# Performance work log

Measured on AMD Instinct MI355X. Metric: run time of the kernel, lower is better.

## Reference

```python
import jax, jax.numpy as jnp
import numpy as np

B, S = 32, 10  # hard-coded in original call()/reshape


def setup_inputs() -> dict:
    key = jax.random.key(0)
    k1, k2, k3 = jax.random.split(key, 3)
    D, K = 4096, 8192
    p = jax.random.normal(k1, (B, S, D), dtype=jnp.float32)
    q = jax.random.normal(k2, (B, S, D), dtype=jnp.float32)
    W = jax.random.uniform(k3, (K, D), dtype=jnp.float32)  # 'uniform' initializer
    return {"p": p, "q": q, "W": W}


def reference(p, q, W):
    # Multi-perspective matching: for each perspective k, weight p rows and the
    # last q state by W[k], then cosine distance = -mean(l2norm(a)*l2norm(b)).
    # Vectorized over (batch, perspective, seq) via einsums on W^2 -- never
    # materializes the (B,K,S,D) weighted tensors.
    D = p.shape[-1]
    W2 = W * W                                   # (K, D)
    q_last = q[:, -1, :]                          # (B, D)
    # dot(w*q_last, w*p_s) = sum_d p*q_last*W^2
    dot = jnp.einsum('bsd,kd->bks', p * q_last[:, None, :], W2)   # (B, K, S)
    norm_p = jnp.sqrt(jnp.einsum('bsd,kd->bks', p * p, W2))       # (B, K, S)
    norm_q = jnp.sqrt(jnp.einsum('bd,kd->bk', q_last * q_last, W2))  # (B, K)
    dist = -dot / (norm_p * norm_q[:, :, None] * D)  # -mean of normalized product
    # original concatenates over k then s per batch, then reshapes to (32,10,K)
    return dist.reshape(B, S, -1)
```

## Files before the change

kernel.cpp:

```cpp
#include <hip/hip_runtime.h>
#include <stdint.h>

#define B_ 32
#define S_ 10
#define D_ 4096
#define K_ 8192
#define RPB 21
#define M_REAL (B_ * RPB)

#define BM 128
#define BN 128
#define BK 32
#define M_PAD_MF 768
#define KSPLIT 2
#define KHALF (D_ / KSPLIT)

typedef _Float16 f16x8 __attribute__((ext_vector_type(8)));
typedef float f32x4 __attribute__((ext_vector_type(4)));
typedef unsigned short us4 __attribute__((ext_vector_type(4)));

__device__ __forceinline__ void async16(const void* g, void* l) {
  __builtin_amdgcn_global_load_lds(
      (const __attribute__((address_space(1))) unsigned int*)g,
      (__attribute__((address_space(3))) unsigned int*)l, 16, 0, 0);
}

__global__ __launch_bounds__(256)
void build_a_f16(const float* __restrict__ p, const float* __restrict__ q,
                 unsigned short* __restrict__ Af) {
  size_t idx = (size_t)blockIdx.x * 256 + threadIdx.x;
  int d4 = (int)(idx & 1023);
  int m = (int)(idx >> 10);
  float4 v = make_float4(0.f, 0.f, 0.f, 0.f);
  if (m < M_REAL) {
    int b = m / RPB;
    int r = m - b * RPB;
    const float4* q4 = (const float4*)(q + (size_t)(b * S_ + (S_ - 1)) * D_);
    if (r < S_) {
      const float4* p4 = (const float4*)(p + (size_t)(b * S_ + r) * D_);
      float4 pv = p4[d4]; float4 qv = q4[d4];
      v = make_float4(pv.x * qv.x, pv.y * qv.y, pv.z * qv.z, pv.w * qv.w);
    } else if (r < 2 * S_) {
      const float4* p4 = (const float4*)(p + (size_t)(b * S_ + (r - S_)) * D_);
      float4 pv = p4[d4];
      v = make_float4(pv.x * pv.x, pv.y * pv.y, pv.z * pv.z, pv.w * pv.w);
    } else {
      float4 qv = q4[d4];
      v = make_float4(qv.x * qv.x, qv.y * qv.y, qv.z * qv.z, qv.w * qv.w);
    }
  }
  us4 h;
  ((unsigned short*)&h)[0] = (unsigned short)__builtin_bit_cast(unsigned short, (_Float16)v.x);
  ((unsigned short*)&h)[1] = (unsigned short)__builtin_bit_cast(unsigned short, (_Float16)v.y);
  ((unsigned short*)&h)[2] = (unsigned short)__builtin_bit_cast(unsigned short, (_Float16)v.z);
  ((unsigned short*)&h)[3] = (unsigned short)__builtin_bit_cast(unsigned short, (_Float16)v.w);
  ((us4*)Af)[idx] = h;
}

__global__ __launch_bounds__(256)
void gemm_mfma(const unsigned short* __restrict__ Af, const float* __restrict__ W,
               float* __restrict__ G) {
  __shared__ unsigned short lds[2 * 128 * 32];
  const int tid = threadIdx.x;
  const int lane = tid & 63;
  const int wid = tid >> 6;
  const int m0 = blockIdx.y * BM;
  const int n0 = blockIdx.x * BN;
  const int ks = blockIdx.z;
  const int d_base = ks * KHALF;

  const unsigned short* gpA[2];
  uint32_t ldsoffA[2];
#pragma unroll
  for (int half = 0; half < 2; ++half) {
    int row = half * 64 + wid * 16 + (lane >> 2);
    int k16l = (lane & 3) ^ ((row ^ (row >> 2)) & 3);
    gpA[half] = Af + (size_t)(m0 + row) * D_ + d_base + k16l * 8;
    ldsoffA[half] = (uint32_t)(half * 4096 + wid * 1024);
  }

  const int wrow = tid >> 1;
  const int wh = tid & 1;
  const float* gW = W + (size_t)(n0 + wrow) * D_ + d_base + wh * 16;
  const int wsz = (wrow ^ (wrow >> 2)) & 3;
  char* const ldsb = (char*)lds;
  char* const ldsWb = ldsb + 8192;
  const uint32_t wbyte0 = (uint32_t)(wrow * 64 + ((2 * wh) ^ wsz) * 16);
  const uint32_t wbyte1 = (uint32_t)(wrow * 64 + ((2 * wh + 1) ^ wsz) * 16);

  f32x4 acc[4][4];
#pragma unroll
  for (int i = 0; i < 4; ++i)
#pragma unroll
    for (int j = 0; j < 4; ++j) acc[i][j] = (f32x4){0.f, 0.f, 0.f, 0.f};

  const int wm = wid >> 1;
  const int wn = wid & 1;
  const int frow = lane & 15;
  const int k16l = lane >> 4;
  int aoff[4], woff[4];
#pragma unroll
  for (int f = 0; f < 4; ++f) {
    int ra = wm * 64 + f * 16 + frow;
    aoff[f] = ra * 64 + ((k16l ^ ((ra ^ (ra >> 2)) & 3)) * 16);
    int rw = wn * 64 + f * 16 + frow;
    woff[f] = rw * 64 + ((k16l ^ ((rw ^ (rw >> 2)) & 3)) * 16);
  }

  for (int d0 = 0; d0 < KHALF; d0 += BK) {
    async16(gpA[0] + d0, ldsb + ldsoffA[0]);
    async16(gpA[1] + d0, ldsb + ldsoffA[1]);
    float4 w0 = *(const float4*)(gW + d0);
    float4 w1 = *(const float4*)(gW + d0 + 4);
    float4 w2 = *(const float4*)(gW + d0 + 8);
    float4 w3 = *(const float4*)(gW + d0 + 12);
    f16x8 o0, o1;
    o0[0] = (_Float16)(w0.x * w0.x); o0[1] = (_Float16)(w0.y * w0.y);
    o0[2] = (_Float16)(w0.z * w0.z); o0[3] = (_Float16)(w0.w * w0.w);
    o0[4] = (_Float16)(w1.x * w1.x); o0[5] = (_Float16)(w1.y * w1.y);
    o0[6] = (_Float16)(w1.z * w1.z); o0[7] = (_Float16)(w1.w * w1.w);
    o1[0] = (_Float16)(w2.x * w2.x); o1[1] = (_Float16)(w2.y * w2.y);
    o1[2] = (_Float16)(w2.z * w2.z); o1[3] = (_Float16)(w2.w * w2.w);
    o1[4] = (_Float16)(w3.x * w3.x); o1[5] = (_Float16)(w3.y * w3.y);
    o1[6] = (_Float16)(w3.z * w3.z); o1[7] = (_Float16)(w3.w * w3.w);
    *(f16x8*)(ldsWb + wbyte0) = o0;
    *(f16x8*)(ldsWb + wbyte1) = o1;
    __syncthreads();

    f16x8 aF[4];
#pragma unroll
    for (int f = 0; f < 4; ++f)
      aF[f] = *(const f16x8*)(ldsb + aoff[f]);
#pragma unroll
    for (int nf = 0; nf < 4; ++nf) {
      f16x8 wF = *(const f16x8*)(ldsWb + woff[nf]);
#pragma unroll
      for (int mf = 0; mf < 4; ++mf)
        acc[mf][nf] = __builtin_amdgcn_mfma_f32_16x16x32_f16(aF[mf], wF, acc[mf][nf], 0, 0, 0);
    }
    __syncthreads();
  }

  float* Gp = G + (size_t)ks * M_PAD_MF * K_;
  const int crow = m0 + wm * 64;
  const int ccol = n0 + wn * 64;
#pragma unroll
  for (int mf = 0; mf < 4; ++mf)
#pragma unroll
    for (int nf = 0; nf < 4; ++nf)
#pragma unroll
      for (int r = 0; r < 4; ++r) {
        int row = crow + mf * 16 + (lane >> 4) * 4 + r;
        int col = ccol + nf * 16 + (lane & 15);
        Gp[(size_t)row * K_ + col] = acc[mf][nf][r];
      }
}

__global__ __launch_bounds__(256)
void epilogue2(const float* __restrict__ G, float* __restrict__ out) {
  __shared__ float buf[256 * S_];
  const int tid = threadIdx.x;
  const int b = blockIdx.y;
  const int k0 = blockIdx.x * 256;
  const int k = k0 + tid;
  const float* G0 = G + (size_t)b * RPB * K_ + k;
  const float* G1 = G0 + (size_t)M_PAD_MF * K_;
  float nq = sqrtf(G0[20 * K_] + G1[20 * K_]);
#pragma unroll
  for (int s = 0; s < S_; ++s) {
    float dot = G0[s * K_] + G1[s * K_];
    float pp = G0[(S_ + s) * K_] + G1[(S_ + s) * K_];
    buf[tid * S_ + s] = -dot / (sqrtf(pp) * nq * (float)D_);
  }
  __syncthreads();
  float* ob = out + ((size_t)b * K_ + k0) * S_;
  for (int i = tid; i < 256 * S_; i += 256) ob[i] = buf[i];
}

extern "C" void kernel_launch(void* const* d_in, const int* in_sizes, int n_in,
                              void* d_out, int out_size, void* d_ws, size_t ws_size,
                              hipStream_t stream) {
  const float* p = (const float*)d_in[0];
  const float* q = (const float*)d_in[1];
  const float* W = (const float*)d_in[2];
  float* out = (float*)d_out;

  uint8_t* w = (uint8_t*)d_ws;
  unsigned short* Af = (unsigned short*)w;
  float* G = (float*)(w + 6291456);

  build_a_f16<<<(M_PAD_MF * (D_ / 4)) / 256, 256, 0, stream>>>(p, q, Af);
  dim3 ggrid(K_ / BN, M_PAD_MF / BM, KSPLIT);
  gemm_mfma<<<ggrid, 256, 0, stream>>>(Af, W, G);
  epilogue2<<<dim3(K_ / 256, B_), 256, 0, stream>>>(G, out);
}
```

Baseline: 104.6 us.

## Double-buffer A tiles and prefetch W registers with BK=64 in MFMA GEMM

Doubles the K-step to 64 and double-buffers the A tile in LDS, issuing the next step's async A loads and W global loads before computing the current step. The W tile stays single-buffered but is written only after a barrier following the MFMAs, so global-load latency overlaps compute. It also switches to an 8-way XOR swizzle and sets a 3-block occupancy hint. The cost is more registers for prefetched W and larger LDS use. Correctness depends on the lgkmcnt wait and barrier ordering around the single W buffer, since the async A writes are tracked by a different counter.

```diff
diff --git a/kernel.cpp b/kernel.cpp
--- a/kernel.cpp
+++ b/kernel.cpp
@@ -10,10 +10,11 @@
 
 #define BM 128
 #define BN 128
-#define BK 32
+#define BK 64
 #define M_PAD_MF 768
 #define KSPLIT 2
 #define KHALF (D_ / KSPLIT)
+#define NSTEP (KHALF / BK)
 
 typedef _Float16 f16x8 __attribute__((ext_vector_type(8)));
 typedef float f32x4 __attribute__((ext_vector_type(4)));
@@ -23,6 +24,15 @@
   __builtin_amdgcn_global_load_lds(
       (const __attribute__((address_space(1))) unsigned int*)g,
       (__attribute__((address_space(3))) unsigned int*)l, 16, 0, 0);
+}
+
+__device__ __forceinline__ f16x8 sqcvt(float4 a, float4 b) {
+  f16x8 o;
+  o[0] = (_Float16)(a.x * a.x); o[1] = (_Float16)(a.y * a.y);
+  o[2] = (_Float16)(a.z * a.z); o[3] = (_Float16)(a.w * a.w);
+  o[4] = (_Float16)(b.x * b.x); o[5] = (_Float16)(b.y * b.y);
+  o[6] = (_Float16)(b.z * b.z); o[7] = (_Float16)(b.w * b.w);
+  return o;
 }
 
 __global__ __launch_bounds__(256)
@@ -57,10 +67,10 @@
   ((us4*)Af)[idx] = h;
 }
 
-__global__ __launch_bounds__(256)
+__global__ __launch_bounds__(256, 3)
 void gemm_mfma(const unsigned short* __restrict__ Af, const float* __restrict__ W,
                float* __restrict__ G) {
-  __shared__ unsigned short lds[2 * 128 * 32];
+  __shared__ unsigned short lds[3 * 128 * 64];
   const int tid = threadIdx.x;
   const int lane = tid & 63;
   const int wid = tid >> 6;
@@ -69,24 +79,27 @@
   const int ks = blockIdx.z;
   const int d_base = ks * KHALF;
 
-  const unsigned short* gpA[2];
-  uint32_t ldsoffA[2];
-#pragma unroll
-  for (int half = 0; half < 2; ++half) {
-    int row = half * 64 + wid * 16 + (lane >> 2);
-    int k16l = (lane & 3) ^ ((row ^ (row >> 2)) & 3);
-    gpA[half] = Af + (size_t)(m0 + row) * D_ + d_base + k16l * 8;
-    ldsoffA[half] = (uint32_t)(half * 4096 + wid * 1024);
+  char* const ldsb = (char*)lds;
+  char* const ldsWb = ldsb + 32768;
+
+  const unsigned short* gpA[4];
+  uint32_t ldsoffA[4];
+#pragma unroll
+  for (int e = 0; e < 4; ++e) {
+    int row = wid * 32 + e * 8 + (lane >> 3);
+    int pc = lane & 7;
+    int c = pc ^ (row & 7);
+    gpA[e] = Af + (size_t)(m0 + row) * D_ + d_base + c * 8;
+    ldsoffA[e] = (uint32_t)((wid * 4 + e) * 1024);
   }
 
   const int wrow = tid >> 1;
   const int wh = tid & 1;
-  const float* gW = W + (size_t)(n0 + wrow) * D_ + d_base + wh * 16;
-  const int wsz = (wrow ^ (wrow >> 2)) & 3;
-  char* const ldsb = (char*)lds;
-  char* const ldsWb = ldsb + 8192;
-  const uint32_t wbyte0 = (uint32_t)(wrow * 64 + ((2 * wh) ^ wsz) * 16);
-  const uint32_t wbyte1 = (uint32_t)(wrow * 64 + ((2 * wh + 1) ^ wsz) * 16);
+  const float* gW = W + (size_t)(n0 + wrow) * D_ + d_base + wh * 32;
+  uint32_t wbyte[4];
+#pragma unroll
+  for (int j = 0; j < 4; ++j)
+    wbyte[j] = (uint32_t)(wrow * 128 + (((wh * 4 + j) ^ (wrow & 7)) * 16));
 
   f32x4 acc[4][4];
 #pragma unroll
@@ -97,47 +110,68 @@
   const int wm = wid >> 1;
   const int wn = wid & 1;
   const int frow = lane & 15;
-  const int k16l = lane >> 4;
-  int aoff[4], woff[4];
-#pragma unroll
-  for (int f = 0; f < 4; ++f) {
-    int ra = wm * 64 + f * 16 + frow;
-    aoff[f] = ra * 64 + ((k16l ^ ((ra ^ (ra >> 2)) & 3)) * 16);
-    int rw = wn * 64 + f * 16 + frow;
-    woff[f] = rw * 64 + ((k16l ^ ((rw ^ (rw >> 2)) & 3)) * 16);
-  }
-
-  for (int d0 = 0; d0 < KHALF; d0 += BK) {
-    async16(gpA[0] + d0, ldsb + ldsoffA[0]);
-    async16(gpA[1] + d0, ldsb + ldsoffA[1]);
-    float4 w0 = *(const float4*)(gW + d0);
-    float4 w1 = *(const float4*)(gW + d0 + 4);
-    float4 w2 = *(const float4*)(gW + d0 + 8);
-    float4 w3 = *(const float4*)(gW + d0 + 12);
-    f16x8 o0, o1;
-    o0[0] = (_Float16)(w0.x * w0.x); o0[1] = (_Float16)(w0.y * w0.y);
-    o0[2] = (_Float16)(w0.z * w0.z); o0[3] = (_Float16)(w0.w * w0.w);
-    o0[4] = (_Float16)(w1.x * w1.x); o0[5] = (_Float16)(w1.y * w1.y);
-    o0[6] = (_Float16)(w1.z * w1.z); o0[7] = (_Float16)(w1.w * w1.w);
-    o1[0] = (_Float16)(w2.x * w2.x); o1[1] = (_Float16)(w2.y * w2.y);
-    o1[2] = (_Float16)(w2.z * w2.z); o1[3] = (_Float16)(w2.w * w2.w);
-    o1[4] = (_Float16)(w3.x * w3.x); o1[5] = (_Float16)(w3.y * w3.y);
-    o1[6] = (_Float16)(w3.z * w3.z); o1[7] = (_Float16)(w3.w * w3.w);
-    *(f16x8*)(ldsWb + wbyte0) = o0;
-    *(f16x8*)(ldsWb + wbyte1) = o1;
-    __syncthreads();
-
-    f16x8 aF[4];
-#pragma unroll
-    for (int f = 0; f < 4; ++f)
-      aF[f] = *(const f16x8*)(ldsb + aoff[f]);
-#pragma unroll
-    for (int nf = 0; nf < 4; ++nf) {
-      f16x8 wF = *(const f16x8*)(ldsWb + woff[nf]);
-#pragma unroll
-      for (int mf = 0; mf < 4; ++mf)
-        acc[mf][nf] = __builtin_amdgcn_mfma_f32_16x16x32_f16(aF[mf], wF, acc[mf][nf], 0, 0, 0);
+  const int k16 = lane >> 4;
+  int aoff[2][4], woff[2][4];
+#pragma unroll
+  for (int kk = 0; kk < 2; ++kk)
+#pragma unroll
+    for (int f = 0; f < 4; ++f) {
+      int ra = wm * 64 + f * 16 + frow;
+      aoff[kk][f] = ra * 128 + (((kk * 4 + k16) ^ (ra & 7)) * 16);
+      int rw = wn * 64 + f * 16 + frow;
+      woff[kk][f] = rw * 128 + (((kk * 4 + k16) ^ (rw & 7)) * 16);
     }
+
+  const float4* gW4 = (const float4*)gW;
+
+  {
+    float4 wv[8];
+#pragma unroll
+    for (int u = 0; u < 8; ++u) wv[u] = gW4[u];
+#pragma unroll
+    for (int e = 0; e < 4; ++e) async16(gpA[e], ldsb + ldsoffA[e]);
+    *(f16x8*)(ldsWb + wbyte[0]) = sqcvt(wv[0], wv[1]);
+    *(f16x8*)(ldsWb + wbyte[1]) = sqcvt(wv[2], wv[3]);
+    *(f16x8*)(ldsWb + wbyte[2]) = sqcvt(wv[4], wv[5]);
+    *(f16x8*)(ldsWb + wbyte[3]) = sqcvt(wv[6], wv[7]);
+  }
+  __syncthreads();
+
+  for (int i = 0; i < NSTEP; ++i) {
+    const int nstep = (i + 1 < NSTEP) ? (i + 1) : i;
+    float4 wv[8];
+#pragma unroll
+    for (int u = 0; u < 8; ++u) wv[u] = gW4[nstep * 16 + u];
+    const uint32_t nb = (uint32_t)(((i + 1) & 1) * 16384);
+#pragma unroll
+    for (int e = 0; e < 4; ++e)
+      async16(gpA[e] + nstep * 64, ldsb + nb + ldsoffA[e]);
+
+    const uint32_t cb = (uint32_t)((i & 1) * 16384);
+#pragma unroll
+    for (int kk = 0; kk < 2; ++kk) {
+      f16x8 aF[4];
+#pragma unroll
+      for (int f = 0; f < 4; ++f)
+        aF[f] = *(const f16x8*)(ldsb + cb + aoff[kk][f]);
+#pragma unroll
+      for (int nf = 0; nf < 4; ++nf) {
+        f16x8 wF = *(const f16x8*)(ldsWb + woff[kk][nf]);
+#pragma unroll
+        for (int mf = 0; mf < 4; ++mf)
+          acc[mf][nf] = __builtin_amdgcn_mfma_f32_16x16x32_f16(aF[mf], wF, acc[mf][nf], 0, 0, 0);
+      }
+    }
+
+    asm volatile("s_waitcnt lgkmcnt(0)" ::: "memory");
+    __builtin_amdgcn_s_barrier();
+    __builtin_amdgcn_sched_barrier(0);
+
+    *(f16x8*)(ldsWb + wbyte[0]) = sqcvt(wv[0], wv[1]);
+    *(f16x8*)(ldsWb + wbyte[1]) = sqcvt(wv[2], wv[3]);
+    *(f16x8*)(ldsWb + wbyte[2]) = sqcvt(wv[4], wv[5]);
+    *(f16x8*)(ldsWb + wbyte[3]) = sqcvt(wv[6], wv[7]);
+
     __syncthreads();
   }
 
```

Result: slower. 146.6 us (+40.2%).

## Double-buffer A and W tiles via async LDS loads, square W from LDS

Applied to the files above, without the earlier changes.

The GEMM main loop now double-buffers both the f16 A tile and the raw fp32 W tile in LDS using global_load_lds, prefetching the next K-step while computing the current one. W is no longer squared and converted in registers before the LDS store. Fragments are read as fp32 from a swizzled LDS layout, then squared and converted to f16 just before the MFMA. This removes one barrier per iteration and overlaps global loads with compute. In exchange LDS use grows to 48KB per block, W's LDS footprint doubles, and the squaring is repeated by both N-warp pairs. The launch bound now asks for 4 blocks per CU.

```diff
diff --git a/kernel.cpp b/kernel.cpp
--- a/kernel.cpp
+++ b/kernel.cpp
@@ -14,6 +14,7 @@
 #define M_PAD_MF 768
 #define KSPLIT 2
 #define KHALF (D_ / KSPLIT)
+#define NSTEP (KHALF / BK)
 
 typedef _Float16 f16x8 __attribute__((ext_vector_type(8)));
 typedef float f32x4 __attribute__((ext_vector_type(4)));
@@ -57,10 +58,10 @@
   ((us4*)Af)[idx] = h;
 }
 
-__global__ __launch_bounds__(256)
+__global__ __launch_bounds__(256, 4)
 void gemm_mfma(const unsigned short* __restrict__ Af, const float* __restrict__ W,
                float* __restrict__ G) {
-  __shared__ unsigned short lds[2 * 128 * 32];
+  __shared__ unsigned short lds[24576];
   const int tid = threadIdx.x;
   const int lane = tid & 63;
   const int wid = tid >> 6;
@@ -69,24 +70,28 @@
   const int ks = blockIdx.z;
   const int d_base = ks * KHALF;
 
+  char* const ldsb = (char*)lds;
+  char* const ldsWf = ldsb + 16384;
+
   const unsigned short* gpA[2];
   uint32_t ldsoffA[2];
 #pragma unroll
   for (int half = 0; half < 2; ++half) {
     int row = half * 64 + wid * 16 + (lane >> 2);
-    int k16l = (lane & 3) ^ ((row ^ (row >> 2)) & 3);
-    gpA[half] = Af + (size_t)(m0 + row) * D_ + d_base + k16l * 8;
+    int g = (lane & 3) ^ ((row ^ (row >> 2)) & 3);
+    gpA[half] = Af + (size_t)(m0 + row) * D_ + d_base + g * 8;
     ldsoffA[half] = (uint32_t)(half * 4096 + wid * 1024);
   }
 
-  const int wrow = tid >> 1;
-  const int wh = tid & 1;
-  const float* gW = W + (size_t)(n0 + wrow) * D_ + d_base + wh * 16;
-  const int wsz = (wrow ^ (wrow >> 2)) & 3;
-  char* const ldsb = (char*)lds;
-  char* const ldsWb = ldsb + 8192;
-  const uint32_t wbyte0 = (uint32_t)(wrow * 64 + ((2 * wh) ^ wsz) * 16);
-  const uint32_t wbyte1 = (uint32_t)(wrow * 64 + ((2 * wh + 1) ^ wsz) * 16);
+  const float* gpW[4];
+  uint32_t ldsoffW[4];
+#pragma unroll
+  for (int e = 0; e < 4; ++e) {
+    int row = wid * 32 + e * 8 + (lane >> 3);
+    int g = (lane & 7) ^ (row & 7);
+    gpW[e] = W + (size_t)(n0 + row) * D_ + d_base + g * 4;
+    ldsoffW[e] = (uint32_t)((wid * 4 + e) * 1024);
+  }
 
   f32x4 acc[4][4];
 #pragma unroll
@@ -97,47 +102,54 @@
   const int wm = wid >> 1;
   const int wn = wid & 1;
   const int frow = lane & 15;
-  const int k16l = lane >> 4;
-  int aoff[4], woff[4];
+  const int k16 = lane >> 4;
+  int aoff[4];
+  int woffL[4], woffH[4];
 #pragma unroll
   for (int f = 0; f < 4; ++f) {
     int ra = wm * 64 + f * 16 + frow;
-    aoff[f] = ra * 64 + ((k16l ^ ((ra ^ (ra >> 2)) & 3)) * 16);
+    aoff[f] = ra * 64 + ((k16 ^ ((ra ^ (ra >> 2)) & 3)) * 16);
     int rw = wn * 64 + f * 16 + frow;
-    woff[f] = rw * 64 + ((k16l ^ ((rw ^ (rw >> 2)) & 3)) * 16);
-  }
-
-  for (int d0 = 0; d0 < KHALF; d0 += BK) {
-    async16(gpA[0] + d0, ldsb + ldsoffA[0]);
-    async16(gpA[1] + d0, ldsb + ldsoffA[1]);
-    float4 w0 = *(const float4*)(gW + d0);
-    float4 w1 = *(const float4*)(gW + d0 + 4);
-    float4 w2 = *(const float4*)(gW + d0 + 8);
-    float4 w3 = *(const float4*)(gW + d0 + 12);
-    f16x8 o0, o1;
-    o0[0] = (_Float16)(w0.x * w0.x); o0[1] = (_Float16)(w0.y * w0.y);
-    o0[2] = (_Float16)(w0.z * w0.z); o0[3] = (_Float16)(w0.w * w0.w);
-    o0[4] = (_Float16)(w1.x * w1.x); o0[5] = (_Float16)(w1.y * w1.y);
-    o0[6] = (_Float16)(w1.z * w1.z); o0[7] = (_Float16)(w1.w * w1.w);
-    o1[0] = (_Float16)(w2.x * w2.x); o1[1] = (_Float16)(w2.y * w2.y);
-    o1[2] = (_Float16)(w2.z * w2.z); o1[3] = (_Float16)(w2.w * w2.w);
-    o1[4] = (_Float16)(w3.x * w3.x); o1[5] = (_Float16)(w3.y * w3.y);
-    o1[6] = (_Float16)(w3.z * w3.z); o1[7] = (_Float16)(w3.w * w3.w);
-    *(f16x8*)(ldsWb + wbyte0) = o0;
-    *(f16x8*)(ldsWb + wbyte1) = o1;
-    __syncthreads();
-
+    woffL[f] = rw * 128 + (((2 * k16) ^ (rw & 7)) * 16);
+    woffH[f] = rw * 128 + (((2 * k16 + 1) ^ (rw & 7)) * 16);
+  }
+
+  async16(gpA[0], ldsb + ldsoffA[0]);
+  async16(gpA[1], ldsb + ldsoffA[1]);
+#pragma unroll
+  for (int e = 0; e < 4; ++e) async16(gpW[e], ldsWf + ldsoffW[e]);
+  __syncthreads();
+
+  for (int i = 0; i < NSTEP; ++i) {
+    const int dn = ((i + 1 < NSTEP) ? (i + 1) : i) * BK;
+    const uint32_t nbA = (uint32_t)(((i + 1) & 1) * 8192);
+    const uint32_t nbW = (uint32_t)(((i + 1) & 1) * 16384);
+    async16(gpA[0] + dn, ldsb + nbA + ldsoffA[0]);
+    async16(gpA[1] + dn, ldsb + nbA + ldsoffA[1]);
+#pragma unroll
+    for (int e = 0; e < 4; ++e)
+      async16(gpW[e] + dn, ldsWf + nbW + ldsoffW[e]);
+
+    const uint32_t cbA = (uint32_t)((i & 1) * 8192);
+    const uint32_t cbW = (uint32_t)((i & 1) * 16384);
     f16x8 aF[4];
 #pragma unroll
     for (int f = 0; f < 4; ++f)
-      aF[f] = *(const f16x8*)(ldsb + aoff[f]);
+      aF[f] = *(const f16x8*)(ldsb + cbA + aoff[f]);
 #pragma unroll
     for (int nf = 0; nf < 4; ++nf) {
-      f16x8 wF = *(const f16x8*)(ldsWb + woff[nf]);
+      f32x4 lo = *(const f32x4*)(ldsWf + cbW + woffL[nf]);
+      f32x4 hi = *(const f32x4*)(ldsWf + cbW + woffH[nf]);
+      f16x8 wF;
+      wF[0] = (_Float16)(lo[0] * lo[0]); wF[1] = (_Float16)(lo[1] * lo[1]);
+      wF[2] = (_Float16)(lo[2] * lo[2]); wF[3] = (_Float16)(lo[3] * lo[3]);
+      wF[4] = (_Float16)(hi[0] * hi[0]); wF[5] = (_Float16)(hi[1] * hi[1]);
+      wF[6] = (_Float16)(hi[2] * hi[2]); wF[7] = (_Float16)(hi[3] * hi[3]);
 #pragma unroll
       for (int mf = 0; mf < 4; ++mf)
         acc[mf][nf] = __builtin_amdgcn_mfma_f32_16x16x32_f16(aF[mf], wF, acc[mf][nf], 0, 0, 0);
     }
+
     __syncthreads();
   }
 
```

Measured after the change: 128.0 us. 22.5% more time.
